# Performance work log

Hardware: AMD Instinct MI355X
Metric: run time of the kernel (lower is better)

## Reference

```python
import jax, jax.numpy as jnp
import numpy as np

BETA = 0.25  # commitment loss weight


def setup_inputs() -> dict:
    key = jax.random.key(0)
    k1, k2 = jax.random.split(key)
    x = jax.random.normal(k1, (16, 2048, 512), dtype=jnp.float32)          # [B, T, D]
    codebooks = jax.random.normal(k2, (8, 1024, 512), dtype=jnp.float32)   # [Q, C, D]
    return {"x": x, "codebooks": codebooks}


def reference(x, codebooks):
    """Residual VQ (SoundStream Algorithm 1): per stage, find nearest codebook
    entry to the current residual (squared-L2 cdist + argmin), gather the code,
    accumulate into the quantized output, subtract from the residual.
    Straight-through estimator on the quantize step; beta-weighted commit loss.
    """

    def step(carry, embed):
        residual, quantized_out, loss = carry  # residual: [B,T,D], embed: [C,D]
        # squared distances ||r - e||^2, GEMM-dominated: [B,T,C]
        d2 = (jnp.sum(residual * residual, axis=-1, keepdims=True)
              - 2.0 * jnp.einsum('btd,cd->btc', residual, embed)
              + jnp.sum(embed * embed, axis=-1))
        idx = jnp.argmin(d2, axis=-1)                 # [B,T] int32
        quant = embed[idx]                            # [B,T,D] gather
        # straight-through: forward value = quant, gradient = identity to residual
        quant_st = residual + jax.lax.stop_gradient(quant - residual)
        loss = loss + BETA * jnp.mean((residual - jax.lax.stop_gradient(quant)) ** 2)
        return (residual - quant_st, quantized_out + quant_st, loss), idx

    init = (x, jnp.zeros_like(x), jnp.float32(0.0))
    (_, quantized_out, loss), all_indices = jax.lax.scan(step, init, codebooks)
    # quantized_out: [B,T,D]; all_indices: [Q,B,T]; loss: scalar
    return quantized_out, all_indices, loss
```

## Files before the change

kernel.cpp:

```cpp
#include <hip/hip_runtime.h>

#define B_   16
#define T_   2048
#define D_   512
#define C_   1024
#define Q_   8
#define M_   (B_ * T_)
#define ND_  (M_ * D_)

static constexpr float BETA = 0.25f;

typedef short  short8v __attribute__((ext_vector_type(8)));
typedef short  short4v __attribute__((ext_vector_type(4)));
typedef float  f32x4   __attribute__((ext_vector_type(4)));

#define WS_CB16     0u
#define WS_ENORM    8388608u
#define WS_IDXI     8421376u
#define WS_FLAGS    8552448u
#define WS_CNT      8683520u
#define WS_NEED1    8683552u
#define WS_CB16LO   8683552u
#define WS_NEED2    17072160u
#define WS_CBT      17072384u
#define WS_NEED3    19169536u
#define WS_NEED3ALL 33849600u

__device__ __forceinline__ short f2bf(float f) {
    unsigned u = __float_as_uint(f);
    u += 0x7fffu + ((u >> 16) & 1u);
    return (short)(u >> 16);
}
__device__ __forceinline__ float bf2f(short s) {
    return __uint_as_float(((unsigned)(unsigned short)s) << 16);
}

__global__ __launch_bounds__(256) void k_enorm(const float* __restrict__ cb,
                                               float* __restrict__ enorm) {
    const int wave = threadIdx.x >> 6;
    const int lane = threadIdx.x & 63;
    const int code = blockIdx.x * 4 + wave;
    const float4* row = (const float4*)(cb + (size_t)code * D_);
    float s = 0.f;
    #pragma unroll
    for (int k = 0; k < 2; ++k) {
        float4 v = row[lane + k * 64];
        s += v.x * v.x + v.y * v.y + v.z * v.z + v.w * v.w;
    }
    #pragma unroll
    for (int m = 32; m; m >>= 1) s += __shfl_xor(s, m);
    if (lane == 0) enorm[code] = s;
}

__global__ __launch_bounds__(256) void k_cvt2f(const float* __restrict__ cb,
                                               short* __restrict__ hi,
                                               short* __restrict__ lo,
                                               int emit_lo) {
    const int idx8 = blockIdx.x * 256 + threadIdx.x;
    const int stage = idx8 >> 16;
    const int g = idx8 & 65535;
    const int lane = g & 63;
    const int h  = lane >> 4, lr = lane & 15;
    const int cj = (g >> 6) & 3;
    const int wc = (g >> 8) & 3;
    const int kb = (g >> 10) & 15;
    const int cc = (g >> 14) & 3;
    const int c  = cc * 256 + wc * 64 + cj * 16 + lr;
    const int ks = kb * 32 + h * 8;
    const float* src = cb + (size_t)stage * (C_ * D_) + (size_t)c * D_ + ks;
    float v[8];
    {
        float4 a = *(const float4*)(src);
        float4 b = *(const float4*)(src + 4);
        v[0]=a.x; v[1]=a.y; v[2]=a.z; v[3]=a.w;
        v[4]=b.x; v[5]=b.y; v[6]=b.z; v[7]=b.w;
    }
    short8v hv, lv;
    #pragma unroll
    for (int k = 0; k < 8; ++k) {
        hv[k] = f2bf(v[k]);
        lv[k] = f2bf(v[k] - bf2f(hv[k]));
    }
    const size_t dst = (size_t)stage * (C_ * D_) + (size_t)g * 8;
    *(short8v*)(hi + dst) = hv;
    if (emit_lo) *(short8v*)(lo + dst) = lv;
}

__global__ __launch_bounds__(64) void k_zero(float* __restrict__ loss,
                                             int* __restrict__ cnt) {
    if (threadIdx.x == 0) *loss = 0.f;
    if (threadIdx.x < 8) cnt[threadIdx.x] = 0;
}

__global__ __launch_bounds__(256)
void k_transpose(const float* __restrict__ cb0, float* __restrict__ cbT0) {
    __shared__ float tile[64][65];
    const float* cbq = cb0 + (size_t)blockIdx.z * C_ * D_;
    float* cbT = cbT0 + (size_t)blockIdx.z * C_ * D_;
    const int tid = threadIdx.x;
    const int c0 = blockIdx.x * 64;
    const int k0 = blockIdx.y * 64;
    #pragma unroll
    for (int i = 0; i < 4; ++i) {
        const int s = tid + i * 256;
        const int r = s >> 4, c4 = s & 15;
        const float4 v = *(const float4*)(cbq + (size_t)(c0 + r) * D_ + k0 + c4 * 4);
        tile[r][c4 * 4 + 0] = v.x; tile[r][c4 * 4 + 1] = v.y;
        tile[r][c4 * 4 + 2] = v.z; tile[r][c4 * 4 + 3] = v.w;
    }
    __syncthreads();
    #pragma unroll
    for (int i = 0; i < 4; ++i) {
        const int s = tid + i * 256;
        const int kk = s >> 4, cc4 = s & 15;
        float4 v;
        v.x = tile[cc4 * 4 + 0][kk]; v.y = tile[cc4 * 4 + 1][kk];
        v.z = tile[cc4 * 4 + 2][kk]; v.w = tile[cc4 * 4 + 3][kk];
        *(float4*)(cbT + (size_t)(k0 + kk) * C_ + c0 + cc4 * 4) = v;
    }
}

#define SA_OFF   0
#define MV1_OFF  131072
#define MV2_OFF  133120
#define MI1_OFF  135168
#define RED_OFF  137216
#define MROW_OFF 137248
#define SM_TOTAL 137760

template <int PLANES>
__global__ __launch_bounds__(512, 2)
void k_approx(const float* __restrict__ x,
              const float* __restrict__ cbprev,
              const short* __restrict__ cb16hi,
              const short* __restrict__ cb16lo,
              const float* __restrict__ enormq,
              float* __restrict__ qout,
              int*   __restrict__ idxi,
              float* __restrict__ idxf,
              int*   __restrict__ flaglist,
              int*   __restrict__ cnt,
              float* __restrict__ loss,
              int q) {
    __shared__ __align__(16) char smem[SM_TOTAL];
    short* smA  = (short*)(smem + SA_OFF);
    float* mv1  = (float*)(smem + MV1_OFF);
    float* mv2  = (float*)(smem + MV2_OFF);
    int*   mi1  = (int*)(smem + MI1_OFF);
    float* red  = (float*)(smem + RED_OFF);
    float* mrow = (float*)(smem + MROW_OFF);

    const int tid  = threadIdx.x;
    const int bid  = blockIdx.x;
    const int lane = tid & 63;
    const int w    = tid >> 6;
    const int rh   = w >> 2;
    const int wc   = w & 3;
    const int h    = lane >> 4;
    const int lr   = lane & 15;
    const int rbase = bid * 128;
    const float slope = (PLANES == 2) ? 0.002f : 0.05f;

    const int prow = tid >> 2;
    const int pqd  = tid & 3;
    const int grow1 = rbase + prow;
    float rn2 = 0.f, rlo2 = 0.f;
    int codep = 0;
    if (q > 0) codep = idxi[grow1];
    #pragma unroll 4
    for (int j = 0; j < 32; ++j) {
        const int c4 = pqd + j * 4;
        const size_t g = (size_t)grow1 * D_ + c4 * 4;
        const float4 xv = *(const float4*)(x + g);
        float4 r;
        if (q == 0) {
            r = xv;
        } else {
            const float4 ev = *(const float4*)(cbprev + (size_t)codep * D_ + c4 * 4);
            float4 nq;
            if (q == 1) nq = ev;
            else {
                const float4 qv = *(const float4*)(qout + g);
                nq = make_float4(qv.x + ev.x, qv.y + ev.y, qv.z + ev.z, qv.w + ev.w);
            }
            *(float4*)(qout + g) = nq;
            r = make_float4(xv.x - nq.x, xv.y - nq.y, xv.z - nq.z, xv.w - nq.w);
        }
        rn2 += r.x * r.x + r.y * r.y + r.z * r.z + r.w * r.w;
        short4v sv; sv[0]=f2bf(r.x); sv[1]=f2bf(r.y); sv[2]=f2bf(r.z); sv[3]=f2bf(r.w);
        const float dx = r.x - bf2f(sv[0]), dy = r.y - bf2f(sv[1]);
        const float dz = r.z - bf2f(sv[2]), dw = r.w - bf2f(sv[3]);
        rlo2 += dx * dx + dy * dy + dz * dz + dw * dw;
        int ab = (prow << 10) + (c4 << 3);
        ab ^= ((prow & 7) << 4);
        *(short4v*)((char*)smA + ab) = sv;
    }
    const float lpart = rn2;
    rn2  += __shfl_xor(rn2, 1);  rn2  += __shfl_xor(rn2, 2);
    rlo2 += __shfl_xor(rlo2, 1); rlo2 += __shfl_xor(rlo2, 2);
    if (pqd == 0)
        mrow[prow] = 32.f * sqrtf(rlo2) + slope * sqrtf(rn2) + 0.05f;
    __syncthreads();
    if (q != 0) {
        float lsum = lpart;
        #pragma unroll
        for (int m = 32; m; m >>= 1) lsum += __shfl_xor(lsum, m);
        if (lane == 0) red[w] = lsum;
        __syncthreads();
        if (tid == 0) {
            float t = 0.f;
            #pragma unroll
            for (int i = 0; i < 8; ++i) t += red[i];
            atomicAdd(loss, t * (BETA / (float)ND_));
        }
    }

    float v1[16], v2[16]; int i1[16];
    #pragma unroll
    for (int i = 0; i < 16; ++i) { v1[i] = 3.4e38f; v2[i] = 3.4e38f; i1[i] = 0; }

    auto bload = [&](const short* __restrict__ src, int cc, int kb, short8v* dst) {
        const short* p = src + (size_t)(((cc * 16 + kb) * 4 + wc) * 4) * 512 + lane * 8;
        #pragma unroll
        for (int cj = 0; cj < 4; ++cj)
            dst[cj] = *(const short8v*)(p + cj * 512);
    };

    short8v b0[4], b1[4];
    bload(cb16hi, 0, 0, b0);
    f32x4 acc[4][4];

    for (int cc = 0; cc < 4; ++cc) {
        #pragma unroll
        for (int ri = 0; ri < 4; ++ri)
            #pragma unroll
            for (int cj = 0; cj < 4; ++cj)
                acc[ri][cj] = (f32x4){0.f, 0.f, 0.f, 0.f};

        if (PLANES == 2) {
            for (int kb = 0; kb < 16; ++kb) {
                bload(cb16lo, cc, kb, b1);
                short8v a[4];
                const int kbyte = kb * 64 + h * 16;
                #pragma unroll
                for (int ri = 0; ri < 4; ++ri) {
                    const int row = rh * 64 + ri * 16 + lr;
                    int off = (row << 10) + kbyte;
                    off ^= ((row & 7) << 4);
                    a[ri] = *(const short8v*)((const char*)smA + off);
                }
                #pragma unroll
                for (int ri = 0; ri < 4; ++ri)
                    #pragma unroll
                    for (int cj = 0; cj < 4; ++cj)
                        acc[ri][cj] = __builtin_amdgcn_mfma_f32_16x16x32_bf16(a[ri], b0[cj], acc[ri][cj], 0, 0, 0);
                const int nkb = (kb == 15) ? 0 : kb + 1;
                const int ncc = (kb == 15) ? (cc < 3 ? cc + 1 : 3) : cc;
                bload(cb16hi, ncc, nkb, b0);
                #pragma unroll
                for (int ri = 0; ri < 4; ++ri)
                    #pragma unroll
                    for (int cj = 0; cj < 4; ++cj)
                        acc[ri][cj] = __builtin_amdgcn_mfma_f32_16x16x32_bf16(a[ri], b1[cj], acc[ri][cj], 0, 0, 0);
            }
        } else {
            for (int kb = 0; kb < 16; kb += 2) {
                {
                    short8v a[4];
                    const int kbyte = kb * 64 + h * 16;
                    #pragma unroll
                    for (int ri = 0; ri < 4; ++ri) {
                        const int row = rh * 64 + ri * 16 + lr;
                        int off = (row << 10) + kbyte;
                        off ^= ((row & 7) << 4);
                        a[ri] = *(const short8v*)((const char*)smA + off);
                    }
                    bload(cb16hi, cc, kb + 1, b1);
                    #pragma unroll
                    for (int ri = 0; ri < 4; ++ri)
                        #pragma unroll
                        for (int cj = 0; cj < 4; ++cj)
                            acc[ri][cj] = __builtin_amdgcn_mfma_f32_16x16x32_bf16(a[ri], b0[cj], acc[ri][cj], 0, 0, 0);
                }
                {
                    short8v a[4];
                    const int kbyte = (kb + 1) * 64 + h * 16;
                    #pragma unroll
                    for (int ri = 0; ri < 4; ++ri) {
                        const int row = rh * 64 + ri * 16 + lr;
                        int off = (row << 10) + kbyte;
                        off ^= ((row & 7) << 4);
                        a[ri] = *(const short8v*)((const char*)smA + off);
                    }
                    const int nkb = (kb == 14) ? 0 : kb + 2;
                    const int ncc = (kb == 14) ? (cc < 3 ? cc + 1 : 3) : cc;
                    bload(cb16hi, ncc, nkb, b0);
                    #pragma unroll
                    for (int ri = 0; ri < 4; ++ri)
                        #pragma unroll
                        for (int cj = 0; cj < 4; ++cj)
                            acc[ri][cj] = __builtin_amdgcn_mfma_f32_16x16x32_bf16(a[ri], b1[cj], acc[ri][cj], 0, 0, 0);
                }
            }
        }

        #pragma unroll
        for (int cj = 0; cj < 4; ++cj) {
            const int codeG = cc * 256 + wc * 64 + cj * 16 + lr;
            const float en = enormq[codeG];
            #pragma unroll
            for (int ri = 0; ri < 4; ++ri)
                #pragma unroll
                for (int rg = 0; rg < 4; ++rg) {
                    const float sv = fmaf(-2.f, acc[ri][cj][rg], en);
                    const int slot = ri * 4 + rg;
                    if (sv < v1[slot]) { v2[slot] = v1[slot]; v1[slot] = sv; i1[slot] = codeG; }
                    else               { v2[slot] = fminf(v2[slot], sv); }
                }
        }
    }

    #pragma unroll
    for (int slot = 0; slot < 16; ++slot) {
        float a1 = v1[slot], a2 = v2[slot]; int ai = i1[slot];
        #pragma unroll
        for (int m = 1; m < 16; m <<= 1) {
            const float b1m = __shfl_xor(a1, m);
            const int   bim = __shfl_xor(ai, m);
            const float b2m = __shfl_xor(a2, m);
            if (b1m < a1 || (b1m == a1 && bim < ai)) { a2 = fminf(a1, b2m); a1 = b1m; ai = bim; }
            else                                     { a2 = fminf(a2, b1m); }
        }
        v1[slot] = a1; v2[slot] = a2; i1[slot] = ai;
    }
    if (lr == 0) {
        #pragma unroll
        for (int ri = 0; ri < 4; ++ri)
            #pragma unroll
            for (int rg = 0; rg < 4; ++rg) {
                const int row = rh * 64 + ri * 16 + h * 4 + rg;
                mv1[wc * 128 + row] = v1[ri * 4 + rg];
                mv2[wc * 128 + row] = v2[ri * 4 + rg];
                mi1[wc * 128 + row] = i1[ri * 4 + rg];
            }
    }
    __syncthreads();

    if (tid < 128) {
        const int row = tid;
        float V1 = mv1[row]; int I1 = mi1[row]; float V2 = mv2[row];
        #pragma unroll
        for (int k = 1; k < 4; ++k) {
            const float b1m = mv1[k * 128 + row];
            const int   bim = mi1[k * 128 + row];
            const float b2m = mv2[k * 128 + row];
            if (b1m < V1 || (b1m == V1 && bim < I1)) { V2 = fminf(V1, b2m); V1 = b1m; I1 = bim; }
            else                                     { V2 = fminf(V2, b1m); }
        }
        const int grow = rbase + row;
        idxi[grow] = I1;
        idxf[grow] = (float)I1;
        if (!(V2 - V1 >= mrow[row])) {
            const int p = atomicAdd(cnt, 1);
            flaglist[p] = grow;
        }
    }
}

__global__ __launch_bounds__(256)
void k_exact_t(const float* __restrict__ x, const float* __restrict__ qout,
               const float* __restrict__ cbT, const float* __restrict__ enq,
               int* __restrict__ idxi, float* __restrict__ idxf,
               const int* __restrict__ flaglist, const int* __restrict__ cnt,
               int useq) {
    __shared__ __align__(16) float rr[8][512];
    __shared__ int   rowid[8];
    __shared__ float wvv[8][4];
    __shared__ int   wii[8][4];
    const int tid  = threadIdx.x;
    const int lane = tid & 63;
    const int wv_  = tid >> 6;
    const int n = *cnt;
    const float4* cbT4 = (const float4*)cbT;

    for (int base = blockIdx.x * 8; base < n; base += gridDim.x * 8) {
        __syncthreads();
        if (tid < 8) rowid[tid] = (base + tid < n) ? flaglist[base + tid] : -1;
        __syncthreads();
        #pragma unroll
        for (int i = 0; i < 4; ++i) {
            const int s = tid + i * 256;
            const int j = s >> 7, k4 = s & 127;
            const int row = rowid[j];
            float4 v = make_float4(0.f, 0.f, 0.f, 0.f);
            if (row >= 0) {
                v = *(const float4*)(x + (size_t)row * D_ + k4 * 4);
                if (useq) {
                    const float4 qv = *(const float4*)(qout + (size_t)row * D_ + k4 * 4);
                    v = make_float4(v.x - qv.x, v.y - qv.y, v.z - qv.z, v.w - qv.w);
                }
            }
            *(float4*)&rr[j][k4 * 4] = v;
        }
        __syncthreads();

        float acc[8][4];
        #pragma unroll
        for (int j = 0; j < 8; ++j)
            #pragma unroll
            for (int c = 0; c < 4; ++c) acc[j][c] = 0.f;

        float4 e0 = cbT4[0 * 256 + tid], e1 = cbT4[1 * 256 + tid];
        float4 e2 = cbT4[2 * 256 + tid], e3 = cbT4[3 * 256 + tid];
        for (int kb = 0; kb < 512; kb += 4) {
            const float4 c0_ = e0, c1_ = e1, c2_ = e2, c3_ = e3;
            if (kb + 4 < 512) {
                e0 = cbT4[(kb + 4) * 256 + tid]; e1 = cbT4[(kb + 5) * 256 + tid];
                e2 = cbT4[(kb + 6) * 256 + tid]; e3 = cbT4[(kb + 7) * 256 + tid];
            }
            #pragma unroll
            for (int j = 0; j < 8; ++j) {
                const float4 rv = *(const float4*)&rr[j][kb];
                acc[j][0] = fmaf(rv.x, c0_.x, acc[j][0]);
                acc[j][1] = fmaf(rv.x, c0_.y, acc[j][1]);
                acc[j][2] = fmaf(rv.x, c0_.z, acc[j][2]);
                acc[j][3] = fmaf(rv.x, c0_.w, acc[j][3]);
                acc[j][0] = fmaf(rv.y, c1_.x, acc[j][0]);
                acc[j][1] = fmaf(rv.y, c1_.y, acc[j][1]);
                acc[j][2] = fmaf(rv.y, c1_.z, acc[j][2]);
                acc[j][3] = fmaf(rv.y, c1_.w, acc[j][3]);
                acc[j][0] = fmaf(rv.z, c2_.x, acc[j][0]);
                acc[j][1] = fmaf(rv.z, c2_.y, acc[j][1]);
                acc[j][2] = fmaf(rv.z, c2_.z, acc[j][2]);
                acc[j][3] = fmaf(rv.z, c2_.w, acc[j][3]);
                acc[j][0] = fmaf(rv.w, c3_.x, acc[j][0]);
                acc[j][1] = fmaf(rv.w, c3_.y, acc[j][1]);
                acc[j][2] = fmaf(rv.w, c3_.z, acc[j][2]);
                acc[j][3] = fmaf(rv.w, c3_.w, acc[j][3]);
            }
        }

        const float4 en4 = *(const float4*)(enq + tid * 4);
        #pragma unroll
        for (int j = 0; j < 8; ++j) {
            float v = 3.4e38f; int id = 0;
            {
                const float s0 = fmaf(-2.f, acc[j][0], en4.x);
                const float s1 = fmaf(-2.f, acc[j][1], en4.y);
                const float s2 = fmaf(-2.f, acc[j][2], en4.z);
                const float s3 = fmaf(-2.f, acc[j][3], en4.w);
                v = s0; id = tid * 4;
                if (s1 < v) { v = s1; id = tid * 4 + 1; }
                if (s2 < v) { v = s2; id = tid * 4 + 2; }
                if (s3 < v) { v = s3; id = tid * 4 + 3; }
            }
            #pragma unroll
            for (int m = 1; m < 64; m <<= 1) {
                const float ov = __shfl_xor(v, m);
                const int  oid = __shfl_xor(id, m);
                if (ov < v || (ov == v && oid < id)) { v = ov; id = oid; }
            }
            if (lane == 0) { wvv[j][wv_] = v; wii[j][wv_] = id; }
        }
        __syncthreads();
        if (tid < 8 && rowid[tid] >= 0) {
            float V = wvv[tid][0]; int I = wii[tid][0];
            #pragma unroll
            for (int k = 1; k < 4; ++k)
                if (wvv[tid][k] < V || (wvv[tid][k] == V && wii[tid][k] < I)) {
                    V = wvv[tid][k]; I = wii[tid][k];
                }
            idxi[rowid[tid]] = I;
            idxf[rowid[tid]] = (float)I;
        }
    }
}

#define XR 4
__global__ __launch_bounds__(256)
void k_exact(const float* __restrict__ x, const float* __restrict__ qout,
             const float* __restrict__ cbq, const float* __restrict__ enq,
             int* __restrict__ idxi, float* __restrict__ idxf,
             const int* __restrict__ flaglist, const int* __restrict__ cnt,
             int useq) {
    __shared__ float rr[XR][512];
    __shared__ int   rowid[XR];
    __shared__ float wv[4];
    __shared__ int   wi[4];
    const int tid = threadIdx.x;
    const int n = *cnt;
    for (int base = blockIdx.x * XR; base < n; base += gridDim.x * XR) {
        __syncthreads();
        if (tid < XR) rowid[tid] = (base + tid < n) ? flaglist[base + tid] : -1;
        __syncthreads();
        #pragma unroll
        for (int i = 0; i < 8; ++i) {
            const int s = tid + i * 256;
            const int j = s >> 9, k = s & 511;
            const int row = rowid[j];
            float v = 0.f;
            if (row >= 0) {
                v = x[(size_t)row * D_ + k];
                if (useq) v -= qout[(size_t)row * D_ + k];
            }
            rr[j][k] = v;
        }
        __syncthreads();
        float dotv[4][XR];
        #pragma unroll
        for (int cs = 0; cs < 4; ++cs)
            #pragma unroll
            for (int j = 0; j < XR; ++j) dotv[cs][j] = 0.f;
        for (int k4 = 0; k4 < 128; ++k4) {
            float4 rv[XR];
            #pragma unroll
            for (int j = 0; j < XR; ++j) rv[j] = *(const float4*)&rr[j][k4 * 4];
            #pragma unroll
            for (int cs = 0; cs < 4; ++cs) {
                const float4 e = *(const float4*)(cbq + (size_t)(cs * 256 + tid) * D_ + k4 * 4);
                #pragma unroll
                for (int j = 0; j < XR; ++j)
                    dotv[cs][j] = fmaf(e.x, rv[j].x, fmaf(e.y, rv[j].y,
                                  fmaf(e.z, rv[j].z, fmaf(e.w, rv[j].w, dotv[cs][j]))));
            }
        }
        float best[XR]; int bidx[XR];
        #pragma unroll
        for (int j = 0; j < XR; ++j) { best[j] = 3.4e38f; bidx[j] = 0; }
        #pragma unroll
        for (int cs = 0; cs < 4; ++cs) {
            const int c = cs * 256 + tid;
            const float en = enq[c];
            #pragma unroll
            for (int j = 0; j < XR; ++j) {
                const float sc = fmaf(-2.f, dotv[cs][j], en);
                if (sc < best[j]) { best[j] = sc; bidx[j] = c; }
            }
        }
        #pragma unroll
        for (int j = 0; j < XR; ++j) {
            float v = best[j]; int id = bidx[j];
            #pragma unroll
            for (int m = 1; m < 64; m <<= 1) {
                const float ov = __shfl_xor(v, m);
                const int  oid = __shfl_xor(id, m);
                if (ov < v || (ov == v && oid < id)) { v = ov; id = oid; }
            }
            if ((tid & 63) == 0) { wv[tid >> 6] = v; wi[tid >> 6] = id; }
            __syncthreads();
            if (tid == 0 && rowid[j] >= 0) {
                float V = wv[0]; int I = wi[0];
                #pragma unroll
                for (int k = 1; k < 4; ++k)
                    if (wv[k] < V || (wv[k] == V && wi[k] < I)) { V = wv[k]; I = wi[k]; }
                idxi[rowid[j]] = I;
                idxf[rowid[j]] = (float)I;
            }
            __syncthreads();
        }
    }
}

__global__ __launch_bounds__(256)
void k_final(const float* __restrict__ x, const float* __restrict__ cb7,
             const int* __restrict__ idxi, float* __restrict__ qout,
             float* __restrict__ loss) {
    __shared__ float red[4];
    const int tid = threadIdx.x;
    const int rbase = blockIdx.x * 64;
    float lsum = 0.f;
    for (int i = 0; i < 32; ++i) {
        const int s = tid + i * 256;
        const int row = s >> 7, c4 = s & 127;
        const int grow = rbase + row;
        const int code = idxi[grow];
        const float4 ev = *(const float4*)(cb7 + (size_t)code * D_ + c4 * 4);
        const size_t g = (size_t)grow * D_ + c4 * 4;
        const float4 xv = *(const float4*)(x + g);
        const float4 qv = *(const float4*)(qout + g);
        const float4 nq = make_float4(qv.x + ev.x, qv.y + ev.y, qv.z + ev.z, qv.w + ev.w);
        *(float4*)(qout + g) = nq;
        const float rx = xv.x - nq.x, ry = xv.y - nq.y;
        const float rz = xv.z - nq.z, rw = xv.w - nq.w;
        lsum += rx * rx + ry * ry + rz * rz + rw * rw;
    }
    #pragma unroll
    for (int m = 32; m; m >>= 1) lsum += __shfl_xor(lsum, m);
    if ((tid & 63) == 0) red[tid >> 6] = lsum;
    __syncthreads();
    if (tid == 0)
        atomicAdd(loss, (red[0] + red[1] + red[2] + red[3]) * (BETA / (float)ND_));
}

__global__ __launch_bounds__(256) void k_init(float* __restrict__ qout,
                                              float* __restrict__ loss) {
    const size_t tid = (size_t)blockIdx.x * blockDim.x + threadIdx.x;
    float4* q4 = (float4*)qout;
    const size_t n4 = ND_ / 4;
    for (size_t i = tid; i < n4; i += (size_t)gridDim.x * blockDim.x)
        q4[i] = make_float4(0.f, 0.f, 0.f, 0.f);
    if (tid == 0) *loss = 0.f;
}

__global__ __launch_bounds__(256) void k_stage(const float* __restrict__ x,
                                               const float* __restrict__ cb,
                                               const float* __restrict__ enorm,
                                               float* __restrict__ qout,
                                               float* __restrict__ idxf,
                                               float* __restrict__ loss) {
    __shared__ float As[16][68];
    __shared__ float Bs[16][68];
    __shared__ int   sidx[64];
    __shared__ float red[4];
    const int tid = threadIdx.x;
    const int ty  = tid >> 4;
    const int tx  = tid & 15;
    const int rbase = blockIdx.x * 64;
    const int lrow = tid >> 2;
    const int ld4  = tid & 3;
    float minv[4]; int mini[4];
    #pragma unroll
    for (int i = 0; i < 4; ++i) { minv[i] = 3.4e38f; mini[i] = 0; }
    for (int cchunk = 0; cchunk < 16; ++cchunk) {
        const int cbase = cchunk * 64;
        float acc[4][4] = {};
        for (int kb = 0; kb < D_; kb += 16) {
            __syncthreads();
            {
                const size_t g = (size_t)(rbase + lrow) * D_ + kb + ld4 * 4;
                const float4 xv = *(const float4*)(x + g);
                const float4 qv = *(const float4*)(qout + g);
                As[ld4*4+0][lrow] = xv.x - qv.x; As[ld4*4+1][lrow] = xv.y - qv.y;
                As[ld4*4+2][lrow] = xv.z - qv.z; As[ld4*4+3][lrow] = xv.w - qv.w;
                const size_t gb = (size_t)(cbase + lrow) * D_ + kb + ld4 * 4;
                const float4 bv = *(const float4*)(cb + gb);
                Bs[ld4*4+0][lrow] = bv.x; Bs[ld4*4+1][lrow] = bv.y;
                Bs[ld4*4+2][lrow] = bv.z; Bs[ld4*4+3][lrow] = bv.w;
            }
            __syncthreads();
            #pragma unroll
            for (int kk = 0; kk < 16; ++kk) {
                const float4 av = *(const float4*)&As[kk][ty * 4];
                const float4 bv = *(const float4*)&Bs[kk][tx * 4];
                const float a[4] = {av.x, av.y, av.z, av.w};
                const float b[4] = {bv.x, bv.y, bv.z, bv.w};
                #pragma unroll
                for (int i = 0; i < 4; ++i)
                    #pragma unroll
                    for (int j = 0; j < 4; ++j)
                        acc[i][j] = fmaf(a[i], b[j], acc[i][j]);
            }
        }
        #pragma unroll
        for (int j = 0; j < 4; ++j) {
            const int c = cbase + tx * 4 + j;
            const float en = enorm[c];
            #pragma unroll
            for (int i = 0; i < 4; ++i) {
                const float s = fmaf(-2.f, acc[i][j], en);
                if (s < minv[i]) { minv[i] = s; mini[i] = c; }
            }
        }
    }
    #pragma unroll
    for (int i = 0; i < 4; ++i) {
        float v = minv[i]; int id = mini[i];
        #pragma unroll
        for (int m = 1; m < 16; m <<= 1) {
            const float ov = __shfl_xor(v, m); const int oid = __shfl_xor(id, m);
            if (ov < v || (ov == v && oid < id)) { v = ov; id = oid; }
        }
        if (tx == 0) sidx[ty * 4 + i] = id;
    }
    __syncthreads();
    if (tid < 64) idxf[rbase + tid] = (float)sidx[tid];
    float lsum = 0.f;
    #pragma unroll 4
    for (int k = 0; k < 32; ++k) {
        const int fidx = tid + k * 256;
        const int row = fidx >> 7, c4 = fidx & 127;
        const int code = sidx[row];
        const float4 qv = *(const float4*)(cb + (size_t)code * D_ + c4 * 4);
        const size_t g = (size_t)(rbase + row) * D_ + c4 * 4;
        const float4 xv = *(const float4*)(x + g);
        const float4 ov = *(const float4*)(qout + g);
        const float4 nq = make_float4(ov.x + qv.x, ov.y + qv.y, ov.z + qv.z, ov.w + qv.w);
        *(float4*)(qout + g) = nq;
        const float rx = xv.x - nq.x, ry = xv.y - nq.y;
        const float rz = xv.z - nq.z, rw = xv.w - nq.w;
        lsum += rx * rx + ry * ry + rz * rz + rw * rw;
    }
    #pragma unroll
    for (int m = 32; m; m >>= 1) lsum += __shfl_xor(lsum, m);
    if ((tid & 63) == 0) red[tid >> 6] = lsum;
    __syncthreads();
    if (tid == 0)
        atomicAdd(loss, (red[0] + red[1] + red[2] + red[3]) * (BETA / (float)ND_));
}

extern "C" void kernel_launch(void* const* d_in, const int* in_sizes, int n_in,
                              void* d_out, int out_size, void* d_ws, size_t ws_size,
                              hipStream_t stream) {
    const float* x  = (const float*)d_in[0];
    const float* cb = (const float*)d_in[1];

    float* out  = (float*)d_out;
    float* qout = out;
    float* idxf = out + (size_t)ND_;
    float* loss = out + (size_t)ND_ + (size_t)Q_ * M_;

    if (ws_size >= WS_NEED1) {
        const bool twop   = (ws_size >= WS_NEED2);
        const bool hascbt = (ws_size >= WS_NEED3);
        const bool hasall = (ws_size >= WS_NEED3ALL);
        char*  ws    = (char*)d_ws;
        short* cb16  = (short*)(ws + WS_CB16);
        short* cb16l = (short*)(ws + WS_CB16LO);
        float* enorm = (float*)(ws + WS_ENORM);
        int*   idxi  = (int*)(ws + WS_IDXI);
        int*   flags = (int*)(ws + WS_FLAGS);
        int*   cnt   = (int*)(ws + WS_CNT);
        float* cbT   = (float*)(ws + WS_CBT);

        hipLaunchKernelGGL(k_zero, dim3(1), dim3(64), 0, stream, loss, cnt);
        hipLaunchKernelGGL(k_cvt2f, dim3(2048), dim3(256), 0, stream,
                           cb, cb16, twop ? cb16l : cb16, twop ? 1 : 0);
        hipLaunchKernelGGL(k_enorm, dim3((Q_ * C_) / 4), dim3(256), 0, stream, cb, enorm);
        if (hasall)
            hipLaunchKernelGGL(k_transpose, dim3(16, 8, 8), dim3(256), 0, stream, cb, cbT);

        for (int q = 0; q < Q_; ++q) {
            if (twop) {
                hipLaunchKernelGGL((k_approx<2>), dim3(M_ / 128), dim3(512), 0, stream,
                                   x, cb + (size_t)(q > 0 ? q - 1 : 0) * C_ * D_,
                                   cb16 + (size_t)q * C_ * D_,
                                   cb16l + (size_t)q * C_ * D_,
                                   enorm + (size_t)q * C_,
                                   qout, idxi, idxf + (size_t)q * M_,
                                   flags, cnt + q, loss, q);
            } else {
                hipLaunchKernelGGL((k_approx<1>), dim3(M_ / 128), dim3(512), 0, stream,
                                   x, cb + (size_t)(q > 0 ? q - 1 : 0) * C_ * D_,
                                   cb16 + (size_t)q * C_ * D_,
                                   cb16 + (size_t)q * C_ * D_,
                                   enorm + (size_t)q * C_,
                                   qout, idxi, idxf + (size_t)q * M_,
                                   flags, cnt + q, loss, q);
            }
            if (hascbt) {
                if (!hasall)
                    hipLaunchKernelGGL(k_transpose, dim3(16, 8, 1), dim3(256), 0, stream,
                                       cb + (size_t)q * C_ * D_, cbT);
                hipLaunchKernelGGL(k_exact_t, dim3(256), dim3(256), 0, stream,
                                   x, qout,
                                   hasall ? (cbT + (size_t)q * C_ * D_) : cbT,
                                   enorm + (size_t)q * C_,
                                   idxi, idxf + (size_t)q * M_,
                                   flags, cnt + q, q > 0 ? 1 : 0);
            } else {
                hipLaunchKernelGGL(k_exact, dim3(512), dim3(256), 0, stream,
                                   x, qout,
                                   cb + (size_t)q * C_ * D_,
                                   enorm + (size_t)q * C_,
                                   idxi, idxf + (size_t)q * M_,
                                   flags, cnt + q, q > 0 ? 1 : 0);
            }
        }
        hipLaunchKernelGGL(k_final, dim3(M_ / 64), dim3(256), 0, stream,
                           x, cb + (size_t)(Q_ - 1) * C_ * D_, idxi, qout, loss);
    } else {
        float* enorm = (float*)d_ws;
        hipLaunchKernelGGL(k_init, dim3(4096), dim3(256), 0, stream, qout, loss);
        hipLaunchKernelGGL(k_enorm, dim3((Q_ * C_) / 4), dim3(256), 0, stream, cb, enorm);
        for (int q = 0; q < Q_; ++q) {
            hipLaunchKernelGGL(k_stage, dim3(M_ / 64), dim3(256), 0, stream,
                               x, cb + (size_t)q * C_ * D_, enorm + (size_t)q * C_,
                               qout, idxf + (size_t)q * M_, loss);
        }
    }
}
```

Baseline: 1.705 ms.

## Split exact re-check over codebook quarters with packed atomicMin argmin

The exact fp32 re-check kernel for flagged rows now uses a 2D grid in which each block covers 256 codes rather than all 1024. Per-block argmin results are merged through a 64-bit atomicMin on an order-preserving packed (distance, index) word, and a new fixup kernel writes the final indices. This spreads the re-check over four times as many blocks and cuts per-thread accumulator registers, at the cost of re-staging each flagged residual four times, atomics, an extra launch, and a new pack buffer that shifts workspace thresholds.

New measurement: 1.602 ms. 1.06x faster.

```diff
diff --git a/kernel.cpp b/kernel.cpp
--- a/kernel.cpp
+++ b/kernel.cpp
@@ -19,12 +19,13 @@
 #define WS_IDXI     8421376u
 #define WS_FLAGS    8552448u
 #define WS_CNT      8683520u
-#define WS_NEED1    8683552u
-#define WS_CB16LO   8683552u
-#define WS_NEED2    17072160u
-#define WS_CBT      17072384u
-#define WS_NEED3    19169536u
-#define WS_NEED3ALL 33849600u
+#define WS_PACK     8683552u
+#define WS_NEED1    8945696u
+#define WS_CB16LO   8945696u
+#define WS_NEED2    17334304u
+#define WS_CBT      17334304u
+#define WS_NEED3    19431456u
+#define WS_NEED3ALL 34111520u
 
 __device__ __forceinline__ short f2bf(float f) {
     unsigned u = __float_as_uint(f);
@@ -33,6 +34,11 @@
 }
 __device__ __forceinline__ float bf2f(short s) {
     return __uint_as_float(((unsigned)(unsigned short)s) << 16);
+}
+__device__ __forceinline__ unsigned long long packSI(float s, int idx) {
+    unsigned u = __float_as_uint(s);
+    u = (u & 0x80000000u) ? ~u : (u | 0x80000000u);
+    return ((unsigned long long)u << 32) | (unsigned)idx;
 }
 
 __global__ __launch_bounds__(256) void k_enorm(const float* __restrict__ cb,
@@ -140,6 +146,7 @@
               float* __restrict__ idxf,
               int*   __restrict__ flaglist,
               int*   __restrict__ cnt,
+              unsigned long long* __restrict__ pack,
               float* __restrict__ loss,
               int q) {
     __shared__ __align__(16) char smem[SM_TOTAL];
@@ -363,16 +370,17 @@
         if (!(V2 - V1 >= mrow[row])) {
             const int p = atomicAdd(cnt, 1);
             flaglist[p] = grow;
+            pack[grow] = ~0ull;
         }
     }
 }
 
 __global__ __launch_bounds__(256)
-void k_exact_t(const float* __restrict__ x, const float* __restrict__ qout,
-               const float* __restrict__ cbT, const float* __restrict__ enq,
-               int* __restrict__ idxi, float* __restrict__ idxf,
-               const int* __restrict__ flaglist, const int* __restrict__ cnt,
-               int useq) {
+void k_exact2(const float* __restrict__ x, const float* __restrict__ qout,
+              const float* __restrict__ cbT, const float* __restrict__ enq,
+              unsigned long long* __restrict__ pack,
+              const int* __restrict__ flaglist, const int* __restrict__ cnt,
+              int useq) {
     __shared__ __align__(16) float rr[8][512];
     __shared__ int   rowid[8];
     __shared__ float wvv[8][4];
@@ -380,8 +388,9 @@
     const int tid  = threadIdx.x;
     const int lane = tid & 63;
     const int wv_  = tid >> 6;
+    const int cglob = blockIdx.y * 256 + tid;
     const int n = *cnt;
-    const float4* cbT4 = (const float4*)cbT;
+    const float* ecol = cbT + cglob;
 
     for (int base = blockIdx.x * 8; base < n; base += gridDim.x * 8) {
         __syncthreads();
@@ -404,56 +413,50 @@
         }
         __syncthreads();
 
-        float acc[8][4];
-        #pragma unroll
-        for (int j = 0; j < 8; ++j)
-            #pragma unroll
-            for (int c = 0; c < 4; ++c) acc[j][c] = 0.f;
-
-        float4 e0 = cbT4[0 * 256 + tid], e1 = cbT4[1 * 256 + tid];
-        float4 e2 = cbT4[2 * 256 + tid], e3 = cbT4[3 * 256 + tid];
-        for (int kb = 0; kb < 512; kb += 4) {
-            const float4 c0_ = e0, c1_ = e1, c2_ = e2, c3_ = e3;
-            if (kb + 4 < 512) {
-                e0 = cbT4[(kb + 4) * 256 + tid]; e1 = cbT4[(kb + 5) * 256 + tid];
-                e2 = cbT4[(kb + 6) * 256 + tid]; e3 = cbT4[(kb + 7) * 256 + tid];
-            }
-            #pragma unroll
-            for (int j = 0; j < 8; ++j) {
-                const float4 rv = *(const float4*)&rr[j][kb];
-                acc[j][0] = fmaf(rv.x, c0_.x, acc[j][0]);
-                acc[j][1] = fmaf(rv.x, c0_.y, acc[j][1]);
-                acc[j][2] = fmaf(rv.x, c0_.z, acc[j][2]);
-                acc[j][3] = fmaf(rv.x, c0_.w, acc[j][3]);
-                acc[j][0] = fmaf(rv.y, c1_.x, acc[j][0]);
-                acc[j][1] = fmaf(rv.y, c1_.y, acc[j][1]);
-                acc[j][2] = fmaf(rv.y, c1_.z, acc[j][2]);
-                acc[j][3] = fmaf(rv.y, c1_.w, acc[j][3]);
-                acc[j][0] = fmaf(rv.z, c2_.x, acc[j][0]);
-                acc[j][1] = fmaf(rv.z, c2_.y, acc[j][1]);
-                acc[j][2] = fmaf(rv.z, c2_.z, acc[j][2]);
-                acc[j][3] = fmaf(rv.z, c2_.w, acc[j][3]);
-                acc[j][0] = fmaf(rv.w, c3_.x, acc[j][0]);
-                acc[j][1] = fmaf(rv.w, c3_.y, acc[j][1]);
-                acc[j][2] = fmaf(rv.w, c3_.z, acc[j][2]);
-                acc[j][3] = fmaf(rv.w, c3_.w, acc[j][3]);
-            }
-        }
-
-        const float4 en4 = *(const float4*)(enq + tid * 4);
+        float acc[8];
+        #pragma unroll
+        for (int j = 0; j < 8; ++j) acc[j] = 0.f;
+
+        float pa[8], pb[8];
+        #pragma unroll
+        for (int t = 0; t < 8; ++t) pa[t] = ecol[(size_t)t * C_];
+        for (int g = 0; g < 64; g += 2) {
+            const int k0 = g * 8;
+            #pragma unroll
+            for (int t = 0; t < 8; ++t) pb[t] = ecol[(size_t)(k0 + 8 + t) * C_];
+            #pragma unroll
+            for (int kk = 0; kk < 8; kk += 4) {
+                #pragma unroll
+                for (int j = 0; j < 8; ++j) {
+                    const float4 rv = *(const float4*)&rr[j][k0 + kk];
+                    acc[j] = fmaf(rv.x, pa[kk + 0], acc[j]);
+                    acc[j] = fmaf(rv.y, pa[kk + 1], acc[j]);
+                    acc[j] = fmaf(rv.z, pa[kk + 2], acc[j]);
+                    acc[j] = fmaf(rv.w, pa[kk + 3], acc[j]);
+                }
+            }
+            if (g + 2 < 64) {
+                #pragma unroll
+                for (int t = 0; t < 8; ++t) pa[t] = ecol[(size_t)(k0 + 16 + t) * C_];
+            }
+            #pragma unroll
+            for (int kk = 0; kk < 8; kk += 4) {
+                #pragma unroll
+                for (int j = 0; j < 8; ++j) {
+                    const float4 rv = *(const float4*)&rr[j][k0 + 8 + kk];
+                    acc[j] = fmaf(rv.x, pb[kk + 0], acc[j]);
+                    acc[j] = fmaf(rv.y, pb[kk + 1], acc[j]);
+                    acc[j] = fmaf(rv.z, pb[kk + 2], acc[j]);
+                    acc[j] = fmaf(rv.w, pb[kk + 3], acc[j]);
+                }
+            }
+        }
+
+        const float en = enq[cglob];
         #pragma unroll
         for (int j = 0; j < 8; ++j) {
-            float v = 3.4e38f; int id = 0;
-            {
-                const float s0 = fmaf(-2.f, acc[j][0], en4.x);
-                const float s1 = fmaf(-2.f, acc[j][1], en4.y);
-                const float s2 = fmaf(-2.f, acc[j][2], en4.z);
-                const float s3 = fmaf(-2.f, acc[j][3], en4.w);
-                v = s0; id = tid * 4;
-                if (s1 < v) { v = s1; id = tid * 4 + 1; }
-                if (s2 < v) { v = s2; id = tid * 4 + 2; }
-                if (s3 < v) { v = s3; id = tid * 4 + 3; }
-            }
+            float v = fmaf(-2.f, acc[j], en);
+            int id = cglob;
             #pragma unroll
             for (int m = 1; m < 64; m <<= 1) {
                 const float ov = __shfl_xor(v, m);
@@ -470,9 +473,21 @@
                 if (wvv[tid][k] < V || (wvv[tid][k] == V && wii[tid][k] < I)) {
                     V = wvv[tid][k]; I = wii[tid][k];
                 }
-            idxi[rowid[tid]] = I;
-            idxf[rowid[tid]] = (float)I;
-        }
+            atomicMin(&pack[rowid[tid]], packSI(V, I));
+        }
+    }
+}
+
+__global__ __launch_bounds__(256)
+void k_fixup(const unsigned long long* __restrict__ pack,
+             const int* __restrict__ flaglist, const int* __restrict__ cnt,
+             int* __restrict__ idxi, float* __restrict__ idxf) {
+    const int n = *cnt;
+    for (int i = blockIdx.x * 256 + threadIdx.x; i < n; i += gridDim.x * 256) {
+        const int row = flaglist[i];
+        const int id = (int)(pack[row] & 0xFFFFFFFFull);
+        idxi[row] = id;
+        idxf[row] = (float)id;
     }
 }
 
@@ -720,6 +735,7 @@
         int*   idxi  = (int*)(ws + WS_IDXI);
         int*   flags = (int*)(ws + WS_FLAGS);
         int*   cnt   = (int*)(ws + WS_CNT);
+        unsigned long long* pack = (unsigned long long*)(ws + WS_PACK);
         float* cbT   = (float*)(ws + WS_CBT);
 
         hipLaunchKernelGGL(k_zero, dim3(1), dim3(64), 0, stream, loss, cnt);
@@ -737,7 +753,7 @@
                                    cb16l + (size_t)q * C_ * D_,
                                    enorm + (size_t)q * C_,
                                    qout, idxi, idxf + (size_t)q * M_,
-                                   flags, cnt + q, loss, q);
+                                   flags, cnt + q, pack, loss, q);
             } else {
                 hipLaunchKernelGGL((k_approx<1>), dim3(M_ / 128), dim3(512), 0, stream,
                                    x, cb + (size_t)(q > 0 ? q - 1 : 0) * C_ * D_,
@@ -745,18 +761,20 @@
                                    cb16 + (size_t)q * C_ * D_,
                                    enorm + (size_t)q * C_,
                                    qout, idxi, idxf + (size_t)q * M_,
-                                   flags, cnt + q, loss, q);
+                                   flags, cnt + q, pack, loss, q);
             }
             if (hascbt) {
                 if (!hasall)
                     hipLaunchKernelGGL(k_transpose, dim3(16, 8, 1), dim3(256), 0, stream,
                                        cb + (size_t)q * C_ * D_, cbT);
-                hipLaunchKernelGGL(k_exact_t, dim3(256), dim3(256), 0, stream,
+                hipLaunchKernelGGL(k_exact2, dim3(256, 4), dim3(256), 0, stream,
                                    x, qout,
                                    hasall ? (cbT + (size_t)q * C_ * D_) : cbT,
                                    enorm + (size_t)q * C_,
-                                   idxi, idxf + (size_t)q * M_,
-                                   flags, cnt + q, q > 0 ? 1 : 0);
+                                   pack, flags, cnt + q, q > 0 ? 1 : 0);
+                hipLaunchKernelGGL(k_fixup, dim3(32), dim3(256), 0, stream,
+                                   pack, flags, cnt + q,
+                                   idxi, idxf + (size_t)q * M_);
             } else {
                 hipLaunchKernelGGL(k_exact, dim3(512), dim3(256), 0, stream,
                                    x, qout,
```
